# Kernel optimization log

Measured on AMD Instinct MI355X. Metric: run time of the kernel, lower is better.

## Reference

```python
import jax, jax.numpy as jnp
import numpy as np

IGNORE_INDEX = -100


def setup_inputs() -> dict:
    key = jax.random.key(0)
    k1, k2, k3 = jax.random.split(key, 3)
    BT, H, V = 2048, 2048, 128000
    x = jax.random.normal(k1, (BT, H), dtype=jnp.float32)
    weight = jax.random.normal(k2, (V, H), dtype=jnp.float32) * (1.0 / np.sqrt(H))
    target = jax.random.randint(k3, (BT,), 0, V, dtype=jnp.int64)
    return {"x": x, "weight": weight, "target": target}


def reference(x, weight, target):
    # Fused linear + cross-entropy forward (reduction='mean').
    # logits: [BT, V], accumulated in fp32 like the helion kernel.
    logits = jnp.einsum("bh,vh->bv", x.astype(jnp.float32), weight.astype(jnp.float32))
    lse = jax.nn.logsumexp(logits, axis=-1)  # [BT]
    target_logit = jnp.take_along_axis(logits, target[:, None], axis=-1)[:, 0]
    valid = (target != IGNORE_INDEX)
    nll = (lse - target_logit) * valid.astype(jnp.float32)  # [BT]
    n_non_ignore = valid.sum().astype(jnp.float32)
    loss = nll.sum() / n_non_ignore
    return loss.astype(x.dtype), lse
```

## Files before the change

### kernel.cpp

```cpp
#include <hip/hip_runtime.h>
#include <hip/hip_bf16.h>


typedef __bf16 bf16x8 __attribute__((ext_vector_type(8)));
typedef float f32x4  __attribute__((ext_vector_type(4)));
typedef float f32x16 __attribute__((ext_vector_type(16)));

#define BM 128
#define BN 128
#define BK 32
#define LDK 40

__device__ __forceinline__ unsigned pkbf(float a, float b) {
  __hip_bfloat162 h = __float22bfloat162_rn(float2{a, b});
  unsigned r;
  __builtin_memcpy(&r, &h, 4);
  return r;
}

__device__ __forceinline__ void gl16(const void* g, const void* l) {
  using GP = const unsigned __attribute__((address_space(1)))*;
  using LP = unsigned __attribute__((address_space(3)))*;
  __builtin_amdgcn_global_load_lds((GP)(unsigned long long)g,
                                   (LP)(unsigned)(unsigned long long)l, 16, 0, 0);
}

#define VM2 asm volatile("s_waitcnt vmcnt(2)" ::: "memory");
#define VM0 asm volatile("s_waitcnt vmcnt(0)" ::: "memory");
#define MEMFENCE asm volatile("" ::: "memory");

__global__ __launch_bounds__(256)
void k_cvt256(const float* __restrict__ src, __bf16* __restrict__ dst, int H, int NT)
{
  const int bid = blockIdx.x;
  const int kt = bid % NT;
  const int r = threadIdx.x;
  const float* s = src + (size_t)((bid / NT) * 256 + r) * H + kt * 64;
  __bf16* d = dst + (size_t)bid * 16384;
  #pragma unroll
  for (int j = 0; j < 8; ++j) {
    float4 f0 = ((const float4*)s)[2 * j];
    float4 f1 = ((const float4*)s)[2 * j + 1];
    uint4 p;
    p.x = pkbf(f0.x, f0.y); p.y = pkbf(f0.z, f0.w);
    p.z = pkbf(f1.x, f1.y); p.w = pkbf(f1.z, f1.w);
    *(uint4*)(d + (j >> 2) * 8192 + (j & 3) * 2048 + r * 8) = p;
  }
}

__global__ __launch_bounds__(256)
void k_tgt(const float* __restrict__ x, const float* __restrict__ w,
           const int* __restrict__ tgt, float* __restrict__ ws_t, int H)
{
  const int row  = blockIdx.x * 4 + (threadIdx.x >> 6);
  const int lane = threadIdx.x & 63;
  const int tv = tgt[row];
  if (tv == -100) { if (lane == 0) ws_t[row] = 0.f; return; }
  const float* xr = x + (size_t)row * H;
  const float* wr = w + (size_t)tv * H;
  float acc = 0.f;
  for (int j = lane * 4; j < H; j += 256) {
    float4 a = *(const float4*)(xr + j);
    float4 b = *(const float4*)(wr + j);
    acc += a.x * b.x + a.y * b.y + a.z * b.z + a.w * b.w;
  }
  #pragma unroll
  for (int m = 1; m < 64; m <<= 1) acc += __shfl_xor(acc, m, 64);
  if (lane == 0) ws_t[row] = acc;
}

__global__ __launch_bounds__(1024, 4)
void k_gemm1024(const __bf16* __restrict__ xb, const __bf16* __restrict__ wb,
                float* __restrict__ ws_m, float* __restrict__ ws_s,
                int S, int NCB, int ROWB)
{
  __shared__ __bf16 As[4][8192];
  __shared__ __bf16 Bs[4][8192];

  int wg = blockIdx.x;
  const int nwg = gridDim.x;
  if ((nwg & 7) == 0) wg = (wg & 7) * (nwg >> 3) + (wg >> 3);
  const int rowb = wg % ROWB;
  const int cb   = wg / ROWB;
  const int row0 = rowb * 256;

  const int t    = threadIdx.x;
  const int lane = t & 63;
  const int wv   = t >> 6;
  const int wr   = wv >> 2;
  const int wc   = wv & 3;

  const int kcoff = (lane >> 4) * 2048;
  const int arow  = wr * 64 + (lane & 15);
  const int bcol  = wc * 64 + (lane & 15);

  const __bf16* ga = xb + (size_t)(rowb * S / 2) * 16384;
  const __bf16* gb = wb + (size_t)(cb * S / 2) * 16384;

  auto stage_slot = [&](int s, int r) {
    const size_t off = (size_t)(s >> 1) * 16384 + (size_t)(s & 1) * 8192
                     + wv * 512 + lane * 8;
    gl16(ga + off, &As[r][wv * 512]);
    gl16(gb + off, &Bs[r][wv * 512]);
  };

  stage_slot(0, 0);
  stage_slot(1, 1);
  VM2
  __builtin_amdgcn_s_barrier();
  MEMFENCE

  f32x4 acc[4][4] = {};

  for (int j = 0; j < S; ++j) {
    const int rj = j & 3;
    if (j + 2 < S) stage_slot(j + 2, (j + 2) & 3);
    bf16x8 aC[4], bC[4];
    #pragma unroll
    for (int m = 0; m < 4; ++m)
      aC[m] = *(const bf16x8*)&As[rj][kcoff + (arow + m * 16) * 8];
    #pragma unroll
    for (int n = 0; n < 4; ++n)
      bC[n] = *(const bf16x8*)&Bs[rj][kcoff + (bcol + n * 16) * 8];
    __builtin_amdgcn_s_setprio(1);
    #pragma unroll
    for (int m = 0; m < 4; ++m)
      #pragma unroll
      for (int n = 0; n < 4; ++n)
        acc[m][n] = __builtin_amdgcn_mfma_f32_16x16x32_bf16(aC[m], bC[n],
                                                            acc[m][n], 0, 0, 0);
    __builtin_amdgcn_s_setprio(0);
    if (j + 2 < S)      { VM2 }
    else if (j + 1 < S) { VM0 }
    if (j + 1 < S) { __builtin_amdgcn_s_barrier(); MEMFENCE }
  }

  __syncthreads();

  float* redM = (float*)&As[0][0];
  float* redS = redM + 1024;
  const int g4 = (lane >> 4) * 4;
  #pragma unroll
  for (int m = 0; m < 4; ++m) {
    #pragma unroll
    for (int r = 0; r < 4; ++r) {
      const int rl = wr * 64 + m * 16 + g4 + r;
      float mx = fmaxf(fmaxf(acc[m][0][r], acc[m][1][r]),
                       fmaxf(acc[m][2][r], acc[m][3][r]));
      #pragma unroll
      for (int sh = 1; sh < 16; sh <<= 1) mx = fmaxf(mx, __shfl_xor(mx, sh, 64));
      float sv = 0.f;
      #pragma unroll
      for (int n = 0; n < 4; ++n) sv += expf(acc[m][n][r] - mx);
      #pragma unroll
      for (int sh = 1; sh < 16; sh <<= 1) sv += __shfl_xor(sv, sh, 64);
      if ((lane & 15) == 0) { redM[wc * 256 + rl] = mx; redS[wc * 256 + rl] = sv; }
    }
  }
  __syncthreads();
  if (t < 256) {
    const float m0 = redM[t], m1 = redM[256 + t], m2 = redM[512 + t], m3 = redM[768 + t];
    float M = fmaxf(fmaxf(m0, m1), fmaxf(m2, m3));
    float S2 = redS[t] * expf(m0 - M) + redS[256 + t] * expf(m1 - M)
             + redS[512 + t] * expf(m2 - M) + redS[768 + t] * expf(m3 - M);
    const int grow = row0 + t;
    ws_m[(size_t)grow * NCB + cb] = M;
    ws_s[(size_t)grow * NCB + cb] = S2;
  }
}

__global__ __launch_bounds__(256, 2)
void k_gemm_lse(const float* __restrict__ x, const float* __restrict__ w,
                const int* __restrict__ tgt,
                float* __restrict__ ws_m, float* __restrict__ ws_s,
                float* __restrict__ ws_t,
                int H, int NCB, int ROWB)
{
  __shared__ unsigned short As[2][BM * LDK];
  __shared__ unsigned short Bs[2][BN * LDK];

  const int bid  = blockIdx.x;
  const int rowb = bid % ROWB;
  const int cb   = bid / ROWB;
  const int row0 = rowb * BM;
  const int col0 = cb * BN;

  const int t    = threadIdx.x;
  const int lane = t & 63;
  const int wv   = t >> 6;
  const int sr = t >> 1;
  const int sk = (t & 1) * 16;

  const float* xa = x + (size_t)(row0 + sr) * H + sk;
  const float* wb = w + (size_t)(col0 + sr) * H + sk;

  float4 ra[4], rb[4];
  #pragma unroll
  for (int i = 0; i < 4; ++i) {
    ra[i] = *(const float4*)(xa + i * 4);
    rb[i] = *(const float4*)(wb + i * 4);
  }

  auto stage = [&](int buf) {
    uint4 p0, p1;
    p0.x = pkbf(ra[0].x, ra[0].y); p0.y = pkbf(ra[0].z, ra[0].w);
    p0.z = pkbf(ra[1].x, ra[1].y); p0.w = pkbf(ra[1].z, ra[1].w);
    p1.x = pkbf(ra[2].x, ra[2].y); p1.y = pkbf(ra[2].z, ra[2].w);
    p1.z = pkbf(ra[3].x, ra[3].y); p1.w = pkbf(ra[3].z, ra[3].w);
    *(uint4*)&As[buf][sr * LDK + sk]     = p0;
    *(uint4*)&As[buf][sr * LDK + sk + 8] = p1;
    p0.x = pkbf(rb[0].x, rb[0].y); p0.y = pkbf(rb[0].z, rb[0].w);
    p0.z = pkbf(rb[1].x, rb[1].y); p0.w = pkbf(rb[1].z, rb[1].w);
    p1.x = pkbf(rb[2].x, rb[2].y); p1.y = pkbf(rb[2].z, rb[2].w);
    p1.z = pkbf(rb[3].x, rb[3].y); p1.w = pkbf(rb[3].z, rb[3].w);
    *(uint4*)&Bs[buf][sr * LDK + sk]     = p0;
    *(uint4*)&Bs[buf][sr * LDK + sk + 8] = p1;
  };

  stage(0);
  __syncthreads();

  f32x16 acc[4] = {};
  const int rlo = lane & 31;
  const int hi  = lane >> 5;
  const int NT  = H / BK;
  int cur = 0;

  for (int kt = 0; kt < NT; ++kt) {
    const bool pf = (kt + 1 < NT);
    if (pf) {
      xa += BK; wb += BK;
      #pragma unroll
      for (int i = 0; i < 4; ++i) {
        ra[i] = *(const float4*)(xa + i * 4);
        rb[i] = *(const float4*)(wb + i * 4);
      }
    }
    const unsigned short* A = As[cur];
    const unsigned short* B = Bs[cur];
    #pragma unroll
    for (int ks = 0; ks < 2; ++ks) {
      const int koff = ks * 16 + hi * 8;
      bf16x8 a = *(const bf16x8*)&A[(wv * 32 + rlo) * LDK + koff];
      #pragma unroll
      for (int nf = 0; nf < 4; ++nf) {
        bf16x8 b = *(const bf16x8*)&B[(nf * 32 + rlo) * LDK + koff];
        acc[nf] = __builtin_amdgcn_mfma_f32_32x32x16_bf16(a, b, acc[nf], 0, 0, 0);
      }
    }
    if (pf) stage(cur ^ 1);
    __syncthreads();
    cur ^= 1;
  }

  #pragma unroll
  for (int reg = 0; reg < 16; ++reg) {
    const int row = wv * 32 + (reg & 3) + 8 * (reg >> 2) + 4 * hi;
    float mx = fmaxf(fmaxf(acc[0][reg], acc[1][reg]), fmaxf(acc[2][reg], acc[3][reg]));
    #pragma unroll
    for (int m = 1; m < 32; m <<= 1) mx = fmaxf(mx, __shfl_xor(mx, m, 64));
    float s = 0.f;
    #pragma unroll
    for (int nf = 0; nf < 4; ++nf) s += expf(acc[nf][reg] - mx);
    #pragma unroll
    for (int m = 1; m < 32; m <<= 1) s += __shfl_xor(s, m, 64);
    const int grow = row0 + row;
    if (rlo == 0) {
      ws_m[(size_t)grow * NCB + cb] = mx;
      ws_s[(size_t)grow * NCB + cb] = s;
    }
    const int tv = tgt[grow];
    #pragma unroll
    for (int nf = 0; nf < 4; ++nf) {
      if (tv == col0 + nf * 32 + rlo) ws_t[grow] = acc[nf][reg];
    }
  }
}

__global__ void k_rowlse(const float* __restrict__ ws_m, const float* __restrict__ ws_s,
                         const float* __restrict__ ws_t, const int* __restrict__ tgt,
                         float* __restrict__ out, float* __restrict__ ws_nll, int NCB)
{
  const int row = blockIdx.x;
  const int t = threadIdx.x;
  const float* pm = ws_m + (size_t)row * NCB;
  const float* ps = ws_s + (size_t)row * NCB;
  __shared__ float red[8];

  float M = -3.0e38f;
  for (int j = t; j < NCB; j += 256) M = fmaxf(M, pm[j]);
  #pragma unroll
  for (int m = 1; m < 64; m <<= 1) M = fmaxf(M, __shfl_xor(M, m, 64));
  if ((t & 63) == 0) red[t >> 6] = M;
  __syncthreads();
  M = fmaxf(fmaxf(red[0], red[1]), fmaxf(red[2], red[3]));

  float S = 0.f;
  for (int j = t; j < NCB; j += 256) S += ps[j] * expf(pm[j] - M);
  #pragma unroll
  for (int m = 1; m < 64; m <<= 1) S += __shfl_xor(S, m, 64);
  if ((t & 63) == 0) red[4 + (t >> 6)] = S;
  __syncthreads();

  if (t == 0) {
    S = red[4] + red[5] + red[6] + red[7];
    const float lse = M + logf(S);
    out[1 + row] = lse;
    const int tv = tgt[row];
    ws_nll[row] = (tv != -100) ? (lse - ws_t[row]) : 0.f;
  }
}

__global__ void k_loss(const float* __restrict__ ws_nll, const int* __restrict__ tgt,
                       float* __restrict__ out, int BT)
{
  const int t = threadIdx.x;
  float s = 0.f, c = 0.f;
  for (int i = t; i < BT; i += 256) {
    s += ws_nll[i];
    c += (tgt[i] != -100) ? 1.f : 0.f;
  }
  __shared__ float rs[4], rc[4];
  #pragma unroll
  for (int m = 1; m < 64; m <<= 1) { s += __shfl_xor(s, m, 64); c += __shfl_xor(c, m, 64); }
  if ((t & 63) == 0) { rs[t >> 6] = s; rc[t >> 6] = c; }
  __syncthreads();
  if (t == 0) {
    s = rs[0] + rs[1] + rs[2] + rs[3];
    c = rc[0] + rc[1] + rc[2] + rc[3];
    out[0] = s / c;
  }
}

extern "C" void kernel_launch(void* const* d_in, const int* in_sizes, int n_in,
                              void* d_out, int out_size, void* d_ws, size_t ws_size,
                              hipStream_t stream)
{
  const float* x  = (const float*)d_in[0];
  const float* w  = (const float*)d_in[1];
  const int* tgt  = (const int*)d_in[2];
  float* out      = (float*)d_out;

  const int BT = in_sizes[2];
  const int H  = in_sizes[0] / BT;
  const int V  = in_sizes[1] / H;

  const int NT    = H / 64;
  const int ROWB  = BT / 256;
  const int NCB   = V / 256;

  const size_t bf_elems   = (size_t)BT * H + (size_t)V * H;
  const size_t need_bytes = bf_elems * 2 + ((size_t)2 * BT * NCB + 2 * (size_t)BT) * 4;

  if (ws_size >= need_bytes && (BT % 256) == 0 && (V % 256) == 0 && (H % 128) == 0) {
    __bf16* x_bf = (__bf16*)d_ws;
    __bf16* w_bf = x_bf + (size_t)BT * H;
    float* ws_m   = (float*)(w_bf + (size_t)V * H);
    float* ws_s   = ws_m + (size_t)BT * NCB;
    float* ws_t   = ws_s + (size_t)BT * NCB;
    float* ws_nll = ws_t + BT;

    k_cvt256<<<(V / 256) * NT, 256, 0, stream>>>(w, w_bf, H, NT);
    k_cvt256<<<(BT / 256) * NT, 256, 0, stream>>>(x, x_bf, H, NT);
    k_tgt<<<BT / 4, 256, 0, stream>>>(x, w, tgt, ws_t, H);
    k_gemm1024<<<ROWB * NCB, 1024, 0, stream>>>(x_bf, w_bf, ws_m, ws_s,
                                                NT * 2, NCB, ROWB);
    k_rowlse<<<BT, 256, 0, stream>>>(ws_m, ws_s, ws_t, tgt, out, ws_nll, NCB);
    k_loss<<<1, 256, 0, stream>>>(ws_nll, tgt, out, BT);
  } else {
    const int ROWB1 = BT / BM;
    const int NCB1  = V / BN;
    float* ws_m   = (float*)d_ws;
    float* ws_s   = ws_m + (size_t)BT * NCB1;
    float* ws_t   = ws_s + (size_t)BT * NCB1;
    float* ws_nll = ws_t + BT;

    k_gemm_lse<<<ROWB1 * NCB1, 256, 0, stream>>>(x, w, tgt, ws_m, ws_s, ws_t, H, NCB1, ROWB1);
    k_rowlse<<<BT, 256, 0, stream>>>(ws_m, ws_s, ws_t, tgt, out, ws_nll, NCB1);
    k_loss<<<1, 256, 0, stream>>>(ws_nll, tgt, out, BT);
  }
}
```

Before: 1.320 ms.

## Use 8-wave GEMM with 128x64 per-wave tiles and phased load/MFMA interleave

Replaces the 16-wave, 1024-thread GEMM with an 8-wave, 512-thread kernel. Each wave now computes a 128x64 output tile with doubled accumulators, and each K-slot is split into two phases that interleave LDS fragment reads, staged global loads and MFMA bursts with barriers. The aim is more register-level reuse of B fragments per LDS read and better overlap of memory traffic with matrix math. In exchange it raises VGPR pressure, which the launch bound of 2 allows for, and adds more barriers per slot.

```diff
diff --git a/kernel.cpp b/kernel.cpp
--- a/kernel.cpp
+++ b/kernel.cpp
@@ -25,8 +25,9 @@
                                    (LP)(unsigned)(unsigned long long)l, 16, 0, 0);
 }
 
-#define VM2 asm volatile("s_waitcnt vmcnt(2)" ::: "memory");
+#define VM4 asm volatile("s_waitcnt vmcnt(4)" ::: "memory");
 #define VM0 asm volatile("s_waitcnt vmcnt(0)" ::: "memory");
+#define NOVM
 #define MEMFENCE asm volatile("" ::: "memory");
 
 __global__ __launch_bounds__(256)
@@ -69,10 +70,50 @@
   if (lane == 0) ws_t[row] = acc;
 }
 
-__global__ __launch_bounds__(1024, 4)
-void k_gemm1024(const __bf16* __restrict__ xb, const __bf16* __restrict__ wb,
-                float* __restrict__ ws_m, float* __restrict__ ws_s,
-                int S, int NCB, int ROWB)
+#define SLOTPH(RJ, DO_ST, STS, VMW)                                            \
+  {                                                                            \
+    _Pragma("unroll")                                                          \
+    for (int m = 0; m < 4; ++m)                                                \
+      aF[m] = *(const bf16x8*)&As[RJ][kcoff + (arow + m * 16) * 8];            \
+    _Pragma("unroll")                                                          \
+    for (int n = 0; n < 4; ++n)                                                \
+      bF[n] = *(const bf16x8*)&Bs[RJ][kcoff + (bcol + n * 16) * 8];            \
+    if (DO_ST) stageA(STS, (STS) & 3);                                         \
+    __builtin_amdgcn_s_barrier();                                              \
+    asm volatile("s_waitcnt lgkmcnt(0)" ::: "memory");                         \
+    __builtin_amdgcn_s_setprio(1);                                             \
+    _Pragma("unroll")                                                          \
+    for (int m = 0; m < 4; ++m)                                                \
+      _Pragma("unroll")                                                        \
+      for (int n = 0; n < 4; ++n)                                              \
+        acc[m][n] = __builtin_amdgcn_mfma_f32_16x16x32_bf16(aF[m], bF[n],      \
+                                                            acc[m][n], 0,0,0); \
+    __builtin_amdgcn_s_setprio(0);                                             \
+    __builtin_amdgcn_s_barrier();                                              \
+    MEMFENCE                                                                   \
+    _Pragma("unroll")                                                          \
+    for (int m = 0; m < 4; ++m)                                                \
+      aF[m] = *(const bf16x8*)&As[RJ][kcoff + (arow + (m + 4) * 16) * 8];      \
+    if (DO_ST) stageB(STS, (STS) & 3);                                         \
+    __builtin_amdgcn_s_barrier();                                              \
+    asm volatile("s_waitcnt lgkmcnt(0)" ::: "memory");                         \
+    __builtin_amdgcn_s_setprio(1);                                             \
+    _Pragma("unroll")                                                          \
+    for (int m = 0; m < 4; ++m)                                                \
+      _Pragma("unroll")                                                        \
+      for (int n = 0; n < 4; ++n)                                              \
+        acc[m + 4][n] = __builtin_amdgcn_mfma_f32_16x16x32_bf16(aF[m], bF[n],  \
+                                                         acc[m + 4][n], 0,0,0);\
+    __builtin_amdgcn_s_setprio(0);                                             \
+    VMW                                                                        \
+    __builtin_amdgcn_s_barrier();                                              \
+    MEMFENCE                                                                   \
+  }
+
+__global__ __launch_bounds__(512, 2)
+void k_gemm_ph(const __bf16* __restrict__ xb, const __bf16* __restrict__ wb,
+               float* __restrict__ ws_m, float* __restrict__ ws_s,
+               int S, int NCB, int ROWB)
 {
   __shared__ __bf16 As[4][8192];
   __shared__ __bf16 Bs[4][8192];
@@ -91,49 +132,45 @@
   const int wc   = wv & 3;
 
   const int kcoff = (lane >> 4) * 2048;
-  const int arow  = wr * 64 + (lane & 15);
+  const int arow  = wr * 128 + (lane & 15);
   const int bcol  = wc * 64 + (lane & 15);
 
-  const __bf16* ga = xb + (size_t)(rowb * S / 2) * 16384;
-  const __bf16* gb = wb + (size_t)(cb * S / 2) * 16384;
-
-  auto stage_slot = [&](int s, int r) {
+  const __bf16* ga = xb + (size_t)(rowb * (S / 2)) * 16384;
+  const __bf16* gb = wb + (size_t)(cb * (S / 2)) * 16384;
+
+  auto stageA = [&](int s, int r) {
     const size_t off = (size_t)(s >> 1) * 16384 + (size_t)(s & 1) * 8192
                      + wv * 512 + lane * 8;
-    gl16(ga + off, &As[r][wv * 512]);
-    gl16(gb + off, &Bs[r][wv * 512]);
+    gl16(ga + off,        &As[r][wv * 512]);
+    gl16(ga + off + 4096, &As[r][4096 + wv * 512]);
   };
-
-  stage_slot(0, 0);
-  stage_slot(1, 1);
-  VM2
+  auto stageB = [&](int s, int r) {
+    const size_t off = (size_t)(s >> 1) * 16384 + (size_t)(s & 1) * 8192
+                     + wv * 512 + lane * 8;
+    gl16(gb + off,        &Bs[r][wv * 512]);
+    gl16(gb + off + 4096, &Bs[r][4096 + wv * 512]);
+  };
+
+  stageA(0, 0); stageB(0, 0);
+  stageA(1, 1); stageB(1, 1);
+  VM4
   __builtin_amdgcn_s_barrier();
   MEMFENCE
 
-  f32x4 acc[4][4] = {};
-
-  for (int j = 0; j < S; ++j) {
-    const int rj = j & 3;
-    if (j + 2 < S) stage_slot(j + 2, (j + 2) & 3);
-    bf16x8 aC[4], bC[4];
-    #pragma unroll
-    for (int m = 0; m < 4; ++m)
-      aC[m] = *(const bf16x8*)&As[rj][kcoff + (arow + m * 16) * 8];
-    #pragma unroll
-    for (int n = 0; n < 4; ++n)
-      bC[n] = *(const bf16x8*)&Bs[rj][kcoff + (bcol + n * 16) * 8];
-    __builtin_amdgcn_s_setprio(1);
-    #pragma unroll
-    for (int m = 0; m < 4; ++m)
-      #pragma unroll
-      for (int n = 0; n < 4; ++n)
-        acc[m][n] = __builtin_amdgcn_mfma_f32_16x16x32_bf16(aC[m], bC[n],
-                                                            acc[m][n], 0, 0, 0);
-    __builtin_amdgcn_s_setprio(0);
-    if (j + 2 < S)      { VM2 }
-    else if (j + 1 < S) { VM0 }
-    if (j + 1 < S) { __builtin_amdgcn_s_barrier(); MEMFENCE }
-  }
+  f32x4 acc[8][4] = {};
+  bf16x8 aF[4], bF[4];
+
+  for (int g = 0; g < (S - 4) / 4; ++g) {
+    const int j0 = g * 4;
+    SLOTPH(0, true, j0 + 2, VM4)
+    SLOTPH(1, true, j0 + 3, VM4)
+    SLOTPH(2, true, j0 + 4, VM4)
+    SLOTPH(3, true, j0 + 5, VM4)
+  }
+  SLOTPH(0, true,  S - 2, VM4)
+  SLOTPH(1, true,  S - 1, VM4)
+  SLOTPH(2, false, 0,     VM0)
+  SLOTPH(3, false, 0,     NOVM)
 
   __syncthreads();
 
@@ -141,10 +178,10 @@
   float* redS = redM + 1024;
   const int g4 = (lane >> 4) * 4;
   #pragma unroll
-  for (int m = 0; m < 4; ++m) {
+  for (int m = 0; m < 8; ++m) {
     #pragma unroll
     for (int r = 0; r < 4; ++r) {
-      const int rl = wr * 64 + m * 16 + g4 + r;
+      const int rl = wr * 128 + m * 16 + g4 + r;
       float mx = fmaxf(fmaxf(acc[m][0][r], acc[m][1][r]),
                        fmaxf(acc[m][2][r], acc[m][3][r]));
       #pragma unroll
@@ -363,8 +400,8 @@
     k_cvt256<<<(V / 256) * NT, 256, 0, stream>>>(w, w_bf, H, NT);
     k_cvt256<<<(BT / 256) * NT, 256, 0, stream>>>(x, x_bf, H, NT);
     k_tgt<<<BT / 4, 256, 0, stream>>>(x, w, tgt, ws_t, H);
-    k_gemm1024<<<ROWB * NCB, 1024, 0, stream>>>(x_bf, w_bf, ws_m, ws_s,
-                                                NT * 2, NCB, ROWB);
+    k_gemm_ph<<<ROWB * NCB, 512, 0, stream>>>(x_bf, w_bf, ws_m, ws_s,
+                                              NT * 2, NCB, ROWB);
     k_rowlse<<<BT, 256, 0, stream>>>(ws_m, ws_s, ws_t, tgt, out, ws_nll, NCB);
     k_loss<<<1, 256, 0, stream>>>(ws_nll, tgt, out, BT);
   } else {
```

New measurement: 1.344 ms. No clear change (+1.8%).
